# Kernel optimization log

Measured on AMD Instinct MI355X. Metric: run time of the kernel, lower is better.

The kernel has to match this reference:

```python
import jax, jax.numpy as jnp
import numpy as np

N = 100_000      # nodes
E = 1_200_000    # edges (avg degree 12)
F_IN = 6         # node_features
H = 64           # hidden_channels
L = 3            # num_layers
EPS = 1e-5       # BatchNorm eps


def setup_inputs() -> dict:
    key = jax.random.key(0)
    ks = jax.random.split(key, 16)
    s = 0.1
    return {
        "x": jax.random.normal(ks[0], (N, F_IN), jnp.float32),
        "edge_index": jax.random.randint(ks[1], (2, E), 0, N, dtype=jnp.int32),
        "edge_attr": jax.random.uniform(ks[2], (E, 1), jnp.float32),
        # node encoder
        "W_enc": jax.random.normal(ks[3], (F_IN, H), jnp.float32) * s,
        "b_enc": jnp.zeros((H,), jnp.float32),
        # per-layer GNN params (stacked over L layers)
        "W_edge": jax.random.normal(ks[4], (L, 1, H), jnp.float32) * s,
        "b_edge": jnp.zeros((L, H), jnp.float32),
        "W_upd": jax.random.normal(ks[5], (L, 2 * H, H), jnp.float32) * s,
        "b_upd": jnp.zeros((L, H), jnp.float32),
        # batch norm (eval mode: running stats)
        "bn_gamma": jnp.ones((L, H), jnp.float32),
        "bn_beta": jnp.zeros((L, H), jnp.float32),
        "bn_mean": jnp.zeros((L, H), jnp.float32),
        "bn_var": jnp.ones((L, H), jnp.float32),
        # path predictor MLP
        "W_p1": jax.random.normal(ks[6], (H, H), jnp.float32) * s,
        "b_p1": jnp.zeros((H,), jnp.float32),
        "W_p2": jax.random.normal(ks[7], (H, 1), jnp.float32) * s,
        "b_p2": jnp.zeros((1,), jnp.float32),
    }


def reference(x, edge_index, edge_attr, W_enc, b_enc, W_edge, b_edge,
              W_upd, b_upd, bn_gamma, bn_beta, bn_mean, bn_var,
              W_p1, b_p1, W_p2, b_p2):
    src, dst = edge_index[0], edge_index[1]  # PyG source_to_target flow
    h = x @ W_enc + b_enc                    # [N, H]
    for i in range(L):
        # message: x_j * lin_edge(edge_attr)
        edge_feat = edge_attr @ W_edge[i] + b_edge[i]      # [E, H]
        msg = h[src] * edge_feat                           # gather + multiply
        # aggregate: scatter-max to target nodes; PyG fills empty rows with 0
        agg = jax.ops.segment_max(msg, dst, num_segments=N)
        agg = jnp.where(jnp.isfinite(agg), agg, 0.0)
        # update: relu(lin_update(cat[x, aggr]))
        h = jax.nn.relu(jnp.concatenate([h, agg], axis=1) @ W_upd[i] + b_upd[i])
        # BatchNorm1d (eval) + relu  (dropout p=0.1 is identity at inference)
        h = (h - bn_mean[i]) * (bn_gamma[i] / jnp.sqrt(bn_var[i] + EPS)) + bn_beta[i]
        h = jax.nn.relu(h)
    # path predictor: Linear -> ReLU -> Linear
    path_scores = jax.nn.relu(h @ W_p1 + b_p1) @ W_p2 + b_p2  # [N, 1]
    return path_scores
```

## Files before the change

kernel.cpp:

```cpp
#include <hip/hip_runtime.h>
#include <hip/hip_fp16.h>

#define FIN 6
#define HC 64
#define LAYERS 3
#define CAP 48
#define ECHUNK 2048

typedef _Float16 f16x8 __attribute__((ext_vector_type(8)));
typedef float f32x4 __attribute__((ext_vector_type(4)));
typedef unsigned int u32x2 __attribute__((ext_vector_type(2)));

__global__ void PathfindingGNN_17274358464713_kernel() {}

__global__ __launch_bounds__(256) void k_enc_scatter(const float* __restrict__ x,
                                                     const float* __restrict__ Wenc,
                                                     const float* __restrict__ benc,
                                                     __half* __restrict__ h16,
                                                     int Nn,
                                                     const int* __restrict__ src,
                                                     const int* __restrict__ dst,
                                                     const float* __restrict__ ea,
                                                     int* __restrict__ counts,
                                                     unsigned int* __restrict__ bucket,
                                                     int E, int edgeB8) {
  if ((int)blockIdx.x < edgeB8) {
    const int part = blockIdx.x & 7;
    const int chunk = blockIdx.x >> 3;
    const int e0 = chunk * ECHUNK;
    const int e1 = min(e0 + ECHUNK, E);
    int dv[8], sv[8];
    float eav[8];
#pragma unroll
    for (int j = 0; j < 8; ++j) {
      int e = e0 + (int)threadIdx.x + j * 256;
      if (e < e1) {
        dv[j] = __builtin_nontemporal_load(&dst[e]);
        sv[j] = __builtin_nontemporal_load(&src[e]);
        eav[j] = __builtin_nontemporal_load(&ea[e]);
      } else {
        dv[j] = -1;
      }
    }
#pragma unroll
    for (int j = 0; j < 8; ++j) {
      int d = dv[j];
      if (d < 0) continue;
      int p8 = (int)(((unsigned int)d * 41u) >> 19);
      if (p8 != part) continue;
      int p = atomicAdd(&counts[d], 1);
      if (p < CAP) {
        unsigned int q = (unsigned int)(eav[j] * 32767.0f + 0.5f);
        bucket[d * CAP + p] = (unsigned int)sv[j] | (q << 17);
      }
    }
    return;
  }
  int idx = (blockIdx.x - edgeB8) * 256 + threadIdx.x;
  if (idx >= Nn * (HC / 4)) return;
  int n = idx >> 4, cp = (idx & 15) * 4;
  float4 bv = *(const float4*)&benc[cp];
  float s0 = bv.x, s1 = bv.y, s2 = bv.z, s3 = bv.w;
#pragma unroll
  for (int f = 0; f < FIN; ++f) {
    float xv = x[n * FIN + f];
    float4 wv = *(const float4*)&Wenc[f * HC + cp];
    s0 = fmaf(xv, wv.x, s0);
    s1 = fmaf(xv, wv.y, s1);
    s2 = fmaf(xv, wv.z, s2);
    s3 = fmaf(xv, wv.w, s3);
  }
  __half2 h01 = __floats2half2_rn(s0, s1);
  __half2 h23 = __floats2half2_rn(s2, s3);
  u32x2 u;
  u.x = *(unsigned int*)&h01;
  u.y = *(unsigned int*)&h23;
  *(u32x2*)&h16[n * HC + cp] = u;
}

__global__ __launch_bounds__(256, 6) void k_layer(const __half* __restrict__ h16,
                                                  const int* __restrict__ counts,
                                                  const unsigned int* __restrict__ bucket,
                                                  const float* __restrict__ We, const float* __restrict__ be,
                                                  const float* __restrict__ W, const float* __restrict__ b,
                                                  const float* __restrict__ gam, const float* __restrict__ bet,
                                                  const float* __restrict__ mean, const float* __restrict__ var,
                                                  __half* __restrict__ out16, int Nn,
                                                  int last, const float* __restrict__ Wp1,
                                                  const float* __restrict__ bp1, const float* __restrict__ Wp2,
                                                  const float* __restrict__ bp2, float* __restrict__ pred) {
  __shared__ alignas(16) __half Wt[64][136];
  __shared__ alignas(16) __half Asm[64][72];

  const int tid = threadIdx.x;
  const int nb = blockIdx.x * 64;
  const int w = tid >> 6;
  const int lr = tid & 15;
  const int lg = (tid >> 4) & 3;
  const float inv15 = 1.0f / 32767.0f;

  int ldn = min(nb + w * 16 + lr, Nn - 1);
  int ldc = min(counts[ldn], CAP);
  const int arow = min(nb + w * 16 + lr, Nn - 1);
  f16x8 aself0 = *(const f16x8*)&h16[arow * HC + lg * 8];
  f16x8 aself1 = *(const f16x8*)&h16[arow * HC + 32 + lg * 8];

  for (int i = tid; i < 128 * 64; i += 256) {
    int k = i >> 6, col = i & 63;
    Wt[col][k] = __float2half(W[i]);
  }

  {
    const int q = (tid >> 4) & 3;
    const int ch0 = (tid & 15) * 4;
    const float4 wev = *(const float4*)&We[ch0];
    const float4 bev = *(const float4*)&be[ch0];

#define PROC(vv, m0, m1, m2, m3) {                                          \
    unsigned int v_ = (vv);                                                 \
    u32x2 hu = *(const u32x2*)&h16[(v_ & 0x1FFFFu) * HC + ch0];             \
    unsigned int hx_ = hu.x, hy_ = hu.y;                                    \
    float qf = (float)(v_ >> 17) * inv15;                                   \
    float2 f01 = __half22float2(*(const __half2*)&hx_);                     \
    float2 f23 = __half22float2(*(const __half2*)&hy_);                     \
    m0 = fmaxf(m0, f01.x * fmaf(qf, wev.x, bev.x));                         \
    m1 = fmaxf(m1, f01.y * fmaf(qf, wev.y, bev.y));                         \
    m2 = fmaxf(m2, f23.x * fmaf(qf, wev.z, bev.z));                         \
    m3 = fmaxf(m3, f23.y * fmaf(qf, wev.w, bev.w)); }

    for (int it = 0; it < 2; ++it) {
      const int iA = q * 4 + it, iB = iA + 2;
      const int nlA = w * 16 + iA, nlB = w * 16 + iB;
      const int cA = __shfl(ldc, iA, 64);
      const int cB = __shfl(ldc, iB, 64);
      const int r0A = min(nb + nlA, Nn - 1) * CAP;
      const int r0B = min(nb + nlB, Nn - 1) * CAP;
      uint4 pa[4], pb[4];
#pragma unroll
      for (int j = 0; j < 4; ++j) pa[j] = *(const uint4*)&bucket[r0A + 4 * j];
#pragma unroll
      for (int j = 0; j < 4; ++j) pb[j] = *(const uint4*)&bucket[r0B + 4 * j];
      float a0 = -INFINITY, a1 = -INFINITY, a2 = -INFINITY, a3 = -INFINITY;
      float b0 = -INFINITY, b1 = -INFINITY, b2 = -INFINITY, b3 = -INFINITY;
#pragma unroll
      for (int j = 0; j < 4; ++j) {
        const int base = 4 * j;
        if (cA > base)     PROC(pa[j].x, a0, a1, a2, a3)
        if (cB > base)     PROC(pb[j].x, b0, b1, b2, b3)
        if (cA > base + 1) PROC(pa[j].y, a0, a1, a2, a3)
        if (cB > base + 1) PROC(pb[j].y, b0, b1, b2, b3)
        if (cA > base + 2) PROC(pa[j].z, a0, a1, a2, a3)
        if (cB > base + 2) PROC(pb[j].z, b0, b1, b2, b3)
        if (cA > base + 3) PROC(pa[j].w, a0, a1, a2, a3)
        if (cB > base + 3) PROC(pb[j].w, b0, b1, b2, b3)
      }
      for (int r = r0A + 16, r1 = r0A + cA; r < r1; ++r) {
        PROC(bucket[r], a0, a1, a2, a3)
      }
      for (int r = r0B + 16, r1 = r0B + cB; r < r1; ++r) {
        PROC(bucket[r], b0, b1, b2, b3)
      }
#define Z(v) ((v == -INFINITY) ? 0.0f : v)
      {
        __half2 h01 = __floats2half2_rn(Z(a0), Z(a1));
        __half2 h23 = __floats2half2_rn(Z(a2), Z(a3));
        u32x2 u;
        u.x = *(unsigned int*)&h01;
        u.y = *(unsigned int*)&h23;
        *(u32x2*)&Asm[nlA][ch0] = u;
      }
      {
        __half2 h01 = __floats2half2_rn(Z(b0), Z(b1));
        __half2 h23 = __floats2half2_rn(Z(b2), Z(b3));
        u32x2 u;
        u.x = *(unsigned int*)&h01;
        u.y = *(unsigned int*)&h23;
        *(u32x2*)&Asm[nlB][ch0] = u;
      }
#undef Z
    }
#undef PROC
  }
  __syncthreads();

  f32x4 acc[4];
#pragma unroll
  for (int t = 0; t < 4; ++t) acc[t] = (f32x4){0.f, 0.f, 0.f, 0.f};
#pragma unroll
  for (int kc = 0; kc < 4; ++kc) {
    const int kof = kc * 32 + lg * 8;
    f16x8 a = (kc == 0) ? aself0
            : (kc == 1) ? aself1
                        : *(const f16x8*)&Asm[w * 16 + lr][kof - 64];
#pragma unroll
    for (int t = 0; t < 4; ++t) {
      f16x8 bf = *(const f16x8*)&Wt[t * 16 + lr][kof];
      acc[t] = __builtin_amdgcn_mfma_f32_16x16x32_f16(a, bf, acc[t], 0, 0, 0);
    }
  }

  float o[4][4];
#pragma unroll
  for (int t = 0; t < 4; ++t) {
    int cc = t * 16 + lr;
    float bias = b[cc];
    float sc = gam[cc] * rsqrtf(var[cc] + 1e-5f);
    float sh = bet[cc] - mean[cc] * sc;
#pragma unroll
    for (int r = 0; r < 4; ++r) {
      float v = fmaxf(acc[t][r] + bias, 0.f);
      o[t][r] = fmaxf(fmaf(v, sc, sh), 0.f);
    }
  }

  const int rbase = nb + w * 16 + lg * 4;
  if (!last) {
#pragma unroll
    for (int r = 0; r < 4; ++r) {
      int n = rbase + r;
      if (n < Nn) {
#pragma unroll
        for (int t = 0; t < 4; ++t)
          out16[n * HC + t * 16 + lr] = __float2half(o[t][r]);
      }
    }
    return;
  }

  __syncthreads();
#pragma unroll
  for (int t = 0; t < 4; ++t)
#pragma unroll
    for (int r = 0; r < 4; ++r)
      Asm[w * 16 + lg * 4 + r][t * 16 + lr] = __float2half(o[t][r]);
  for (int i = tid; i < 64 * 64; i += 256) {
    int k = i >> 6, col = i & 63;
    Wt[col][k] = __float2half(Wp1[i]);
  }
  __syncthreads();

  f32x4 acc2[4];
#pragma unroll
  for (int t = 0; t < 4; ++t) acc2[t] = (f32x4){0.f, 0.f, 0.f, 0.f};
#pragma unroll
  for (int kc = 0; kc < 2; ++kc) {
    const int kof = kc * 32 + lg * 8;
    f16x8 a = *(const f16x8*)&Asm[w * 16 + lr][kof];
#pragma unroll
    for (int t = 0; t < 4; ++t) {
      f16x8 bf = *(const f16x8*)&Wt[t * 16 + lr][kof];
      acc2[t] = __builtin_amdgcn_mfma_f32_16x16x32_f16(a, bf, acc2[t], 0, 0, 0);
    }
  }

  float s[4] = {0.f, 0.f, 0.f, 0.f};
#pragma unroll
  for (int t = 0; t < 4; ++t) {
    int cc = t * 16 + lr;
    float b1 = bp1[cc], w2 = Wp2[cc];
#pragma unroll
    for (int r = 0; r < 4; ++r) {
      float pv = fmaxf(acc2[t][r] + b1, 0.f);
      s[r] = fmaf(pv, w2, s[r]);
    }
  }
#pragma unroll
  for (int msk = 1; msk < 16; msk <<= 1) {
#pragma unroll
    for (int r = 0; r < 4; ++r) s[r] += __shfl_xor(s[r], msk, 64);
  }
  if (lr == 0) {
    float b2 = bp2[0];
#pragma unroll
    for (int r = 0; r < 4; ++r) {
      int n = rbase + r;
      if (n < Nn) pred[n] = s[r] + b2;
    }
  }
}

extern "C" void kernel_launch(void* const* d_in, const int* in_sizes, int n_in,
                              void* d_out, int out_size, void* d_ws, size_t ws_size,
                              hipStream_t stream) {
  const float* x = (const float*)d_in[0];
  const int* eidx = (const int*)d_in[1];
  const float* eattr = (const float*)d_in[2];
  const float* Wenc = (const float*)d_in[3];
  const float* benc = (const float*)d_in[4];
  const float* Wedge = (const float*)d_in[5];
  const float* bedge = (const float*)d_in[6];
  const float* Wupd = (const float*)d_in[7];
  const float* bupd = (const float*)d_in[8];
  const float* bng = (const float*)d_in[9];
  const float* bnb = (const float*)d_in[10];
  const float* bnm = (const float*)d_in[11];
  const float* bnv = (const float*)d_in[12];
  const float* Wp1 = (const float*)d_in[13];
  const float* bp1 = (const float*)d_in[14];
  const float* Wp2 = (const float*)d_in[15];
  const float* bp2 = (const float*)d_in[16];

  const int Nn = in_sizes[0] / FIN;
  const int E = in_sizes[1] / 2;
  const int* src = eidx;
  const int* dst = eidx + E;
  const int NH = Nn * HC;

  size_t off = 0;
  char* base = (char*)d_ws;
  auto carve = [&](size_t bytes) -> void* {
    void* p = base + off;
    off += (bytes + 255) & ~(size_t)255;
    return p;
  };
  int* counts = (int*)carve((size_t)Nn * 4);
  unsigned int* bucket = (unsigned int*)carve((size_t)Nn * CAP * 4);
  __half* hA16 = (__half*)carve((size_t)NH * 2);
  __half* hB16 = (__half*)carve((size_t)NH * 2);
  if (off > ws_size) return;

  int nhB = (Nn * (HC / 4) + 255) / 256;
  int edgeB8 = 8 * ((E + ECHUNK - 1) / ECHUNK);
  int updB = (Nn + 63) / 64;

  hipMemsetAsync(counts, 0, (size_t)Nn * 4, stream);
  k_enc_scatter<<<edgeB8 + nhB, 256, 0, stream>>>(x, Wenc, benc, hA16, Nn,
                                                  src, dst, eattr, counts, bucket, E, edgeB8);

  __half* hc16 = hA16;
  __half* hn16 = hB16;
  for (int i = 0; i < LAYERS; ++i) {
    int last = (i == LAYERS - 1) ? 1 : 0;
    k_layer<<<updB, 256, 0, stream>>>(hc16, counts, bucket,
                                      Wedge + i * HC, bedge + i * HC,
                                      Wupd + i * 2 * HC * HC, bupd + i * HC,
                                      bng + i * HC, bnb + i * HC, bnm + i * HC, bnv + i * HC,
                                      hn16, Nn,
                                      last, Wp1, bp1, Wp2, bp2, (float*)d_out);
    __half* t16 = hc16; hc16 = hn16; hn16 = t16;
  }
}
```

Baseline: 351.6 us.

## Bin edges into partition queues once, then scatter per partition; gather four nodes at once

The edge bucketing is split into two passes. The first kernel reads each edge once and uses shared-memory counters and one global atomic per partition per block to append packed 64-bit (dst, src, quantized attr) records into 8 partition queues. A second kernel walks each queue and does the per-node atomic bucket insert, so atomics stay within one node range. This replaces the old scheme, where every edge chunk was reread by 8 blocks. Separately, the layer's max-aggregation now interleaves 4 destination nodes per thread instead of two passes of 2, for more memory-level parallelism at the cost of higher register pressure under the 6-wave launch bound. The queue reuses the second hidden buffer as scratch.

```diff
diff --git a/kernel.cpp b/kernel.cpp
--- a/kernel.cpp
+++ b/kernel.cpp
@@ -13,27 +13,30 @@
 
 __global__ void PathfindingGNN_17274358464713_kernel() {}
 
-__global__ __launch_bounds__(256) void k_enc_scatter(const float* __restrict__ x,
-                                                     const float* __restrict__ Wenc,
-                                                     const float* __restrict__ benc,
-                                                     __half* __restrict__ h16,
-                                                     int Nn,
-                                                     const int* __restrict__ src,
-                                                     const int* __restrict__ dst,
-                                                     const float* __restrict__ ea,
-                                                     int* __restrict__ counts,
-                                                     unsigned int* __restrict__ bucket,
-                                                     int E, int edgeB8) {
-  if ((int)blockIdx.x < edgeB8) {
-    const int part = blockIdx.x & 7;
-    const int chunk = blockIdx.x >> 3;
-    const int e0 = chunk * ECHUNK;
+__global__ __launch_bounds__(256) void k_part_enc(const float* __restrict__ x,
+                                                  const float* __restrict__ Wenc,
+                                                  const float* __restrict__ benc,
+                                                  __half* __restrict__ h16,
+                                                  int Nn,
+                                                  const int* __restrict__ src,
+                                                  const int* __restrict__ dst,
+                                                  const float* __restrict__ ea,
+                                                  int* __restrict__ qcount,
+                                                  unsigned long long* __restrict__ queue,
+                                                  int qcap, int E, int edgeB) {
+  if ((int)blockIdx.x < edgeB) {
+    __shared__ int lcnt[8];
+    __shared__ int gbase[8];
+    const int tid = threadIdx.x;
+    if (tid < 8) lcnt[tid] = 0;
+    __syncthreads();
+    const int e0 = blockIdx.x * ECHUNK;
     const int e1 = min(e0 + ECHUNK, E);
-    int dv[8], sv[8];
+    int dv[8], sv[8], pv[8], lp[8];
     float eav[8];
 #pragma unroll
     for (int j = 0; j < 8; ++j) {
-      int e = e0 + (int)threadIdx.x + j * 256;
+      int e = e0 + tid + j * 256;
       if (e < e1) {
         dv[j] = __builtin_nontemporal_load(&dst[e]);
         sv[j] = __builtin_nontemporal_load(&src[e]);
@@ -44,19 +47,31 @@
     }
 #pragma unroll
     for (int j = 0; j < 8; ++j) {
-      int d = dv[j];
-      if (d < 0) continue;
-      int p8 = (int)(((unsigned int)d * 41u) >> 19);
-      if (p8 != part) continue;
-      int p = atomicAdd(&counts[d], 1);
-      if (p < CAP) {
-        unsigned int q = (unsigned int)(eav[j] * 32767.0f + 0.5f);
-        bucket[d * CAP + p] = (unsigned int)sv[j] | (q << 17);
+      if (dv[j] >= 0) {
+        pv[j] = (int)(((unsigned int)dv[j] * 41u) >> 19);
+        lp[j] = atomicAdd(&lcnt[pv[j]], 1);
       }
     }
+    __syncthreads();
+    if (tid < 8) gbase[tid] = atomicAdd(&qcount[tid], lcnt[tid]);
+    __syncthreads();
+#pragma unroll
+    for (int j = 0; j < 8; ++j) {
+      if (dv[j] >= 0) {
+        int p = pv[j];
+        int idx = gbase[p] + lp[j];
+        if (idx < qcap) {
+          unsigned int q = (unsigned int)(eav[j] * 32767.0f + 0.5f);
+          unsigned long long rec =
+              (unsigned long long)((unsigned int)sv[j] | (q << 17)) |
+              ((unsigned long long)(unsigned int)dv[j] << 32);
+          queue[(size_t)p * qcap + idx] = rec;
+        }
+      }
+    }
     return;
   }
-  int idx = (blockIdx.x - edgeB8) * 256 + threadIdx.x;
+  int idx = (blockIdx.x - edgeB) * 256 + threadIdx.x;
   if (idx >= Nn * (HC / 4)) return;
   int n = idx >> 4, cp = (idx & 15) * 4;
   float4 bv = *(const float4*)&benc[cp];
@@ -76,6 +91,29 @@
   u.x = *(unsigned int*)&h01;
   u.y = *(unsigned int*)&h23;
   *(u32x2*)&h16[n * HC + cp] = u;
+}
+
+__global__ __launch_bounds__(256) void k_scatter(const int* __restrict__ qcount,
+                                                 const unsigned long long* __restrict__ queue,
+                                                 int* __restrict__ counts,
+                                                 unsigned int* __restrict__ bucket,
+                                                 int qcap) {
+  const int part = blockIdx.x & 7;
+  const int chunk = blockIdx.x >> 3;
+  const int n = min(qcount[part], qcap);
+  const int base = chunk * 2048 + (int)threadIdx.x;
+  const unsigned long long* qp = queue + (size_t)part * qcap;
+#pragma unroll
+  for (int j = 0; j < 8; ++j) {
+    int i = base + j * 256;
+    if (i < n) {
+      unsigned long long rec = __builtin_nontemporal_load(&qp[i]);
+      int d = (int)(rec >> 32);
+      unsigned int sq = (unsigned int)rec;
+      int pos = atomicAdd(&counts[d], 1);
+      if (pos < CAP) bucket[d * CAP + pos] = sq;
+    }
+  }
 }
 
 __global__ __launch_bounds__(256, 6) void k_layer(const __half* __restrict__ h16,
@@ -101,7 +139,7 @@
 
   int ldn = min(nb + w * 16 + lr, Nn - 1);
   int ldc = min(counts[ldn], CAP);
-  const int arow = min(nb + w * 16 + lr, Nn - 1);
+  const int arow = ldn;
   f16x8 aself0 = *(const f16x8*)&h16[arow * HC + lg * 8];
   f16x8 aself1 = *(const f16x8*)&h16[arow * HC + 32 + lg * 8];
 
@@ -128,58 +166,62 @@
     m2 = fmaxf(m2, f23.x * fmaf(qf, wev.z, bev.z));                         \
     m3 = fmaxf(m3, f23.y * fmaf(qf, wev.w, bev.w)); }
 
-    for (int it = 0; it < 2; ++it) {
-      const int iA = q * 4 + it, iB = iA + 2;
-      const int nlA = w * 16 + iA, nlB = w * 16 + iB;
-      const int cA = __shfl(ldc, iA, 64);
-      const int cB = __shfl(ldc, iB, 64);
-      const int r0A = min(nb + nlA, Nn - 1) * CAP;
-      const int r0B = min(nb + nlB, Nn - 1) * CAP;
-      uint4 pa[4], pb[4];
-#pragma unroll
-      for (int j = 0; j < 4; ++j) pa[j] = *(const uint4*)&bucket[r0A + 4 * j];
-#pragma unroll
-      for (int j = 0; j < 4; ++j) pb[j] = *(const uint4*)&bucket[r0B + 4 * j];
-      float a0 = -INFINITY, a1 = -INFINITY, a2 = -INFINITY, a3 = -INFINITY;
-      float b0 = -INFINITY, b1 = -INFINITY, b2 = -INFINITY, b3 = -INFINITY;
-#pragma unroll
-      for (int j = 0; j < 4; ++j) {
-        const int base = 4 * j;
-        if (cA > base)     PROC(pa[j].x, a0, a1, a2, a3)
-        if (cB > base)     PROC(pb[j].x, b0, b1, b2, b3)
-        if (cA > base + 1) PROC(pa[j].y, a0, a1, a2, a3)
-        if (cB > base + 1) PROC(pb[j].y, b0, b1, b2, b3)
-        if (cA > base + 2) PROC(pa[j].z, a0, a1, a2, a3)
-        if (cB > base + 2) PROC(pb[j].z, b0, b1, b2, b3)
-        if (cA > base + 3) PROC(pa[j].w, a0, a1, a2, a3)
-        if (cB > base + 3) PROC(pb[j].w, b0, b1, b2, b3)
-      }
-      for (int r = r0A + 16, r1 = r0A + cA; r < r1; ++r) {
-        PROC(bucket[r], a0, a1, a2, a3)
-      }
-      for (int r = r0B + 16, r1 = r0B + cB; r < r1; ++r) {
-        PROC(bucket[r], b0, b1, b2, b3)
-      }
-#define Z(v) ((v == -INFINITY) ? 0.0f : v)
-      {
-        __half2 h01 = __floats2half2_rn(Z(a0), Z(a1));
-        __half2 h23 = __floats2half2_rn(Z(a2), Z(a3));
-        u32x2 u;
-        u.x = *(unsigned int*)&h01;
-        u.y = *(unsigned int*)&h23;
-        *(u32x2*)&Asm[nlA][ch0] = u;
-      }
-      {
-        __half2 h01 = __floats2half2_rn(Z(b0), Z(b1));
-        __half2 h23 = __floats2half2_rn(Z(b2), Z(b3));
-        u32x2 u;
-        u.x = *(unsigned int*)&h01;
-        u.y = *(unsigned int*)&h23;
-        *(u32x2*)&Asm[nlB][ch0] = u;
-      }
-#undef Z
-    }
+    int cn0 = __shfl(ldc, q * 4 + 0, 64);
+    int cn1 = __shfl(ldc, q * 4 + 1, 64);
+    int cn2 = __shfl(ldc, q * 4 + 2, 64);
+    int cn3 = __shfl(ldc, q * 4 + 3, 64);
+    const int r00 = min(nb + w * 16 + q * 4 + 0, Nn - 1) * CAP;
+    const int r01 = min(nb + w * 16 + q * 4 + 1, Nn - 1) * CAP;
+    const int r02 = min(nb + w * 16 + q * 4 + 2, Nn - 1) * CAP;
+    const int r03 = min(nb + w * 16 + q * 4 + 3, Nn - 1) * CAP;
+    uint4 p0[4], p1[4], p2[4], p3[4];
+#pragma unroll
+    for (int j = 0; j < 4; ++j) p0[j] = *(const uint4*)&bucket[r00 + 4 * j];
+#pragma unroll
+    for (int j = 0; j < 4; ++j) p1[j] = *(const uint4*)&bucket[r01 + 4 * j];
+#pragma unroll
+    for (int j = 0; j < 4; ++j) p2[j] = *(const uint4*)&bucket[r02 + 4 * j];
+#pragma unroll
+    for (int j = 0; j < 4; ++j) p3[j] = *(const uint4*)&bucket[r03 + 4 * j];
+    float m0[4], m1[4], m2[4], m3[4];
+#pragma unroll
+    for (int i = 0; i < 4; ++i) { m0[i] = -INFINITY; m1[i] = -INFINITY; m2[i] = -INFINITY; m3[i] = -INFINITY; }
+#pragma unroll
+    for (int j = 0; j < 4; ++j) {
+      const int base = 4 * j;
+      if (cn0 > base)     PROC(p0[j].x, m0[0], m0[1], m0[2], m0[3])
+      if (cn1 > base)     PROC(p1[j].x, m1[0], m1[1], m1[2], m1[3])
+      if (cn2 > base)     PROC(p2[j].x, m2[0], m2[1], m2[2], m2[3])
+      if (cn3 > base)     PROC(p3[j].x, m3[0], m3[1], m3[2], m3[3])
+      if (cn0 > base + 1) PROC(p0[j].y, m0[0], m0[1], m0[2], m0[3])
+      if (cn1 > base + 1) PROC(p1[j].y, m1[0], m1[1], m1[2], m1[3])
+      if (cn2 > base + 1) PROC(p2[j].y, m2[0], m2[1], m2[2], m2[3])
+      if (cn3 > base + 1) PROC(p3[j].y, m3[0], m3[1], m3[2], m3[3])
+      if (cn0 > base + 2) PROC(p0[j].z, m0[0], m0[1], m0[2], m0[3])
+      if (cn1 > base + 2) PROC(p1[j].z, m1[0], m1[1], m1[2], m1[3])
+      if (cn2 > base + 2) PROC(p2[j].z, m2[0], m2[1], m2[2], m2[3])
+      if (cn3 > base + 2) PROC(p3[j].z, m3[0], m3[1], m3[2], m3[3])
+      if (cn0 > base + 3) PROC(p0[j].w, m0[0], m0[1], m0[2], m0[3])
+      if (cn1 > base + 3) PROC(p1[j].w, m1[0], m1[1], m1[2], m1[3])
+      if (cn2 > base + 3) PROC(p2[j].w, m2[0], m2[1], m2[2], m2[3])
+      if (cn3 > base + 3) PROC(p3[j].w, m3[0], m3[1], m3[2], m3[3])
+    }
+    for (int r = r00 + 16, r1 = r00 + cn0; r < r1; ++r) PROC(bucket[r], m0[0], m0[1], m0[2], m0[3])
+    for (int r = r01 + 16, r1 = r01 + cn1; r < r1; ++r) PROC(bucket[r], m1[0], m1[1], m1[2], m1[3])
+    for (int r = r02 + 16, r1 = r02 + cn2; r < r1; ++r) PROC(bucket[r], m2[0], m2[1], m2[2], m2[3])
+    for (int r = r03 + 16, r1 = r03 + cn3; r < r1; ++r) PROC(bucket[r], m3[0], m3[1], m3[2], m3[3])
 #undef PROC
+#define STORE(mm, i) {                                                      \
+    __half2 h01 = __floats2half2_rn((mm[0] == -INFINITY) ? 0.f : mm[0],     \
+                                    (mm[1] == -INFINITY) ? 0.f : mm[1]);    \
+    __half2 h23 = __floats2half2_rn((mm[2] == -INFINITY) ? 0.f : mm[2],     \
+                                    (mm[3] == -INFINITY) ? 0.f : mm[3]);    \
+    u32x2 u;                                                                \
+    u.x = *(unsigned int*)&h01;                                             \
+    u.y = *(unsigned int*)&h23;                                             \
+    *(u32x2*)&Asm[w * 16 + q * 4 + i][ch0] = u; }
+    STORE(m0, 0) STORE(m1, 1) STORE(m2, 2) STORE(m3, 3)
+#undef STORE
   }
   __syncthreads();
 
@@ -313,19 +355,25 @@
     off += (bytes + 255) & ~(size_t)255;
     return p;
   };
-  int* counts = (int*)carve((size_t)Nn * 4);
+  int* counts = (int*)carve((size_t)(Nn + 8) * 4);
   unsigned int* bucket = (unsigned int*)carve((size_t)Nn * CAP * 4);
   __half* hA16 = (__half*)carve((size_t)NH * 2);
   __half* hB16 = (__half*)carve((size_t)NH * 2);
   if (off > ws_size) return;
 
+  int* qcount = counts + Nn;
+  unsigned long long* queue = (unsigned long long*)hB16;
+  const int qcap = Nn * 2;
+
   int nhB = (Nn * (HC / 4) + 255) / 256;
-  int edgeB8 = 8 * ((E + ECHUNK - 1) / ECHUNK);
+  int edgeB = (E + ECHUNK - 1) / ECHUNK;
   int updB = (Nn + 63) / 64;
-
-  hipMemsetAsync(counts, 0, (size_t)Nn * 4, stream);
-  k_enc_scatter<<<edgeB8 + nhB, 256, 0, stream>>>(x, Wenc, benc, hA16, Nn,
-                                                  src, dst, eattr, counts, bucket, E, edgeB8);
+  int schunks = (qcap + 2047) / 2048;
+
+  hipMemsetAsync(counts, 0, (size_t)(Nn + 8) * 4, stream);
+  k_part_enc<<<edgeB + nhB, 256, 0, stream>>>(x, Wenc, benc, hA16, Nn,
+                                              src, dst, eattr, qcount, queue, qcap, E, edgeB);
+  k_scatter<<<8 * schunks, 256, 0, stream>>>(qcount, queue, counts, bucket, qcap);
 
   __half* hc16 = hA16;
   __half* hn16 = hB16;
```

Result: slower. 430.7 us (+22.5%).
